# Kernel optimization log

Measured on AMD Instinct MI355X. Metric: run time of the kernel, lower is better.

Reference implementation:

```python
import jax, jax.numpy as jnp
import numpy as np

DIMS = [14400, 7200, 3600, 1800, 900, 450]  # in_dim then floor(dim/2) per layer
K = 25
BATCH = 256
NSTEPS = 10
OUT_DIM = 2


def setup_inputs() -> dict:
    key = jax.random.key(0)
    ks = jax.random.split(key, 13)
    inp = {"input": jax.random.normal(ks[0], (BATCH, NSTEPS, DIMS[0]), dtype=jnp.float32)}
    w_scale = (2.0 / K) ** 0.5  # matches normal_(0, (2/K)**0.5) init
    for i in range(5):
        d_prev, d = DIMS[i], DIMS[i + 1]
        inp[f"knn{i}"] = jax.random.randint(ks[1 + i], (d, K), 0, d_prev)
        inp[f"w{i}"] = w_scale * jax.random.normal(ks[6 + i], (d, K), dtype=jnp.float32)
        inp[f"b{i}"] = jnp.zeros((1, d), dtype=jnp.float32)
    inp["fc_w"] = jax.random.normal(ks[11], (OUT_DIM, DIMS[-1]), dtype=jnp.float32) * (1.0 / DIMS[-1] ** 0.5)
    inp["fc_b"] = jnp.zeros((OUT_DIM,), dtype=jnp.float32)
    return inp


def reference(input, knn0, knn1, knn2, knn3, knn4,
              w0, w1, w2, w3, w4, b0, b1, b2, b3, b4, fc_w, fc_b):
    # Faithful to the torch module: the synapses/membranes dicts are never
    # reassigned inside the step loop, so every snntorch Synaptic call sees
    # zero state: reset = Heaviside(0 - thr) = 0, syn = alpha*0 + I = I,
    # mem = beta*0 + syn = I.  The returned mem (x) is therefore exactly the
    # layer drive, there is no cross-step recurrence, and `angles` is
    # overwritten each step, so only the final timestep reaches the output.
    knns = (knn0, knn1, knn2, knn3, knn4)
    ws = (w0, w1, w2, w3, w4)
    bs = (b0, b1, b2, b3, b4)
    x = input[:, -1, :]  # [B, in_dim] -- last step (permute(1,0,2) then input[step])
    for knn, w, b in zip(knns, ws, bs):
        # gather KNN inputs [B, dim, K], weight locally, reduce over K, add bias
        x = jnp.einsum('bdk,dk->bd', x[:, knn], w) + b
    angles = x @ fc_w.T + fc_b  # fc_angle
    return angles  # (mem4_rec, spk4_rec are empty lists in the original)
```

## Files before the change

### kernel.cpp

```cpp
#include <hip/hip_runtime.h>

#define NSTEPS 10
#define D_IN   14400
#define KNN_K  25

#define L0D 7200
#define L1D 3600
#define L2D 1800
#define L3D 900
#define L4D 450
#define NROWS 13950

#define G0 113
#define G1 57
#define G2 29
#define G3 15
#define G4 8
#define SPG 832
#define O1 (G0*SPG)
#define O2 (O1 + G1*SPG)
#define O3 (O2 + G2*SPG)
#define O4 (O3 + G3*SPG)
#define OTOT (O4 + G4*SPG)

#define NPAIR 128
#define NPACK (NPAIR * (D_IN/4))

#define SPLIT0 3584

__device__ __forceinline__ unsigned bf16b(float x) {
    unsigned u = __float_as_uint(x);
    return (u + 0x7fffu + ((u >> 16) & 1u)) >> 16;
}

__device__ __forceinline__ void gpairB(unsigned u, const char* __restrict__ actb,
                                       float& s0, float& s1) {
    unsigned av = *(const unsigned*)(actb + (u & 0xffffu));
    float wf = __uint_as_float(u & 0xffff0000u);
    s0 = fmaf(__uint_as_float(av << 16),          wf, s0);
    s1 = fmaf(__uint_as_float(av & 0xffff0000u),  wf, s1);
}

__global__ void prep_kernel(const int* __restrict__ k0, const float* __restrict__ w0,
                            const int* __restrict__ k1, const float* __restrict__ w1,
                            const int* __restrict__ k2, const float* __restrict__ w2,
                            const int* __restrict__ k3, const float* __restrict__ w3,
                            const int* __restrict__ k4, const float* __restrict__ w4,
                            const float* __restrict__ input,
                            uint2* __restrict__ tile, uint4* __restrict__ xpk)
{
    const int s = blockIdx.x * 256 + threadIdx.x;
    if (s < NROWS) {
        const int* kp; const float* wp; int dl, obase;
        if      (s < L0D)             { kp = k0; wp = w0; dl = s;         obase = 0;  }
        else if (s < L0D+L1D)         { kp = k1; wp = w1; dl = s - L0D;   obase = O1; }
        else if (s < L0D+L1D+L2D)     { kp = k2; wp = w2; dl = s-L0D-L1D; obase = O2; }
        else if (s < L0D+L1D+L2D+L3D) { kp = k3; wp = w3; dl = s-L0D-L1D-L2D; obase = O3; }
        else                          { kp = k4; wp = w4; dl = s-L0D-L1D-L2D-L3D; obase = O4; }
        const int g = dl >> 6, l = dl & 63;

        int   idx[KNN_K]; float wv[KNN_K]; int bk[KNN_K];
#pragma unroll
        for (int k = 0; k < KNN_K; ++k) {
            idx[k] = kp[dl * KNN_K + k];
            wv[k]  = wp[dl * KNN_K + k];
            bk[k]  = idx[k] & 31;
        }
        const int lm = l - (l >= 50 ? 50 : (l >= 25 ? 25 : 0));
        unsigned* tw = (unsigned*)tile + 2u * (unsigned)(obase + g * SPG);
#pragma unroll
        for (int k = 0; k < KNN_K; ++k) {
            int rank = 0;
#pragma unroll
            for (int j = 0; j < KNN_K; ++j)
                rank += (bk[j] < bk[k]) || (bk[j] == bk[k] && j < k);
            int slot = rank + lm; if (slot >= KNN_K) slot -= KNN_K;
            unsigned u = (bf16b(wv[k]) << 16) | ((unsigned)idx[k] << 2);
            tw[((slot >> 1) * 64 + l) * 2 + (slot & 1)] = u;
        }
        tw[(12 * 64 + l) * 2 + 1] = 0;
        return;
    }
    const int t = s - NROWS;
    if (t < NPACK) {
        const int p = t / (D_IN / 4);
        const int c = t - p * (D_IN / 4);
        const float4 a = *(const float4*)(input + ((size_t)(2*p)   * NSTEPS + NSTEPS-1) * D_IN + 4*c);
        const float4 b = *(const float4*)(input + ((size_t)(2*p+1) * NSTEPS + NSTEPS-1) * D_IN + 4*c);
        uint4 wd;
        wd.x = bf16b(a.x) | (bf16b(b.x) << 16);
        wd.y = bf16b(a.y) | (bf16b(b.y) << 16);
        wd.z = bf16b(a.z) | (bf16b(b.z) << 16);
        wd.w = bf16b(a.w) | (bf16b(b.w) << 16);
        xpk[(size_t)p * (D_IN / 4) + c] = wd;
    }
}

__global__ __launch_bounds__(512, 2)
void lcn_l0(const uint4* __restrict__ xpk, const uint2* __restrict__ tile,
            const float* __restrict__ bias0, unsigned* __restrict__ y0)
{
    __shared__ unsigned act[D_IN];
    const int tid = threadIdx.x;
    const int p   = blockIdx.x & 127;
    const int h   = blockIdx.x >> 7;

    const uint4* src = xpk + (size_t)p * (D_IN / 4);
    for (int i = tid; i < D_IN / 4; i += 512)
        *(uint4*)(act + i * 4) = src[i];
    __syncthreads();
    const char* actb = (const char*)act;

    const int rbase = h ? SPLIT0 : 0;
    const int rend  = h ? L0D    : SPLIT0;
#pragma unroll
    for (int i = 0; i < 8; ++i) {
        int r = rbase + tid + i * 512;
        if (r < rend) {
            const uint2* tp = tile + (size_t)(r >> 6) * SPG + (r & 63);
            float a = bias0[r], b = a, c = 0.f, d = 0.f;
#pragma unroll
            for (int j = 0; j < 13; ++j) {
                uint2 u = tp[j * 64];
                gpairB(u.x, actb, a, b);
                gpairB(u.y, actb, c, d);
            }
            a += c; b += d;
            y0[(size_t)p * L0D + r] = bf16b(a) | (bf16b(b) << 16);
        }
    }
}

template<int DIM>
__device__ __forceinline__ void glayerT(const char* __restrict__ actb,
                                        unsigned* __restrict__ yout,
                                        const uint2* __restrict__ tb,
                                        const float* __restrict__ bias, int tid)
{
#pragma unroll
    for (int i = 0; i < (DIM + 1023) / 1024; ++i) {
        int r = tid + i * 1024;
        if (r < DIM) {
            const uint2* tp = tb + (size_t)(r >> 6) * SPG + (r & 63);
            float a = bias[r], b = a, c = 0.f, d = 0.f;
#pragma unroll
            for (int j = 0; j < 13; ++j) {
                uint2 u = tp[j * 64];
                gpairB(u.x, actb, a, b);
                gpairB(u.y, actb, c, d);
            }
            a += c; b += d;
            yout[r] = bf16b(a) | (bf16b(b) << 16);
        }
    }
}

__global__ __launch_bounds__(1024)
void lcn_tail(const unsigned* __restrict__ y0, const uint2* __restrict__ tile,
              const float* __restrict__ b1, const float* __restrict__ b2,
              const float* __restrict__ b3, const float* __restrict__ b4,
              const float* __restrict__ fc_w, const float* __restrict__ fc_b,
              float* __restrict__ out)
{
    __shared__ unsigned sm[L0D + L1D];
    const int tid = threadIdx.x;
    const int p   = blockIdx.x;

    const uint4* src = (const uint4*)(y0 + (size_t)p * L0D);
    for (int i = tid; i < L0D / 4; i += 1024)
        *(uint4*)(sm + 4 * i) = src[i];
    __syncthreads();

    glayerT<L1D>((const char*)sm,         sm + L0D,        tile + O1, b1, tid);
    __syncthreads();
    glayerT<L2D>((const char*)(sm + L0D), sm,              tile + O2, b2, tid);
    __syncthreads();
    glayerT<L3D>((const char*)sm,         sm + L2D,        tile + O3, b3, tid);
    __syncthreads();
    glayerT<L4D>((const char*)(sm + L2D), sm + L2D + L3D,  tile + O4, b4, tid);
    __syncthreads();

    const unsigned* C = sm + L2D + L3D;
    if (tid < 256) {
        const int wv = tid >> 6, lane = tid & 63;
        const int o = wv >> 1, j = wv & 1;
        float s = 0.f;
#pragma unroll
        for (int it = 0; it < 8; ++it) {
            int r = lane + it * 64;
            if (r < L4D) {
                unsigned av = C[r];
                unsigned hbits = j ? (av & 0xffff0000u) : (av << 16);
                s += __uint_as_float(hbits) * fc_w[o * L4D + r];
            }
        }
#pragma unroll
        for (int off = 32; off > 0; off >>= 1) s += __shfl_xor(s, off);
        if (lane == 0) out[(2 * p + j) * 2 + o] = s + fc_b[o];
    }
}

extern "C" void kernel_launch(void* const* d_in, const int* in_sizes, int n_in,
                              void* d_out, int out_size, void* d_ws, size_t ws_size,
                              hipStream_t stream) {
    const float* input = (const float*)d_in[0];
    const int*   knn[5];
    const float* w[5];
    const float* bias[5];
    for (int i = 0; i < 5; ++i) {
        knn[i]  = (const int*)  d_in[1 + 3 * i];
        w[i]    = (const float*)d_in[2 + 3 * i];
        bias[i] = (const float*)d_in[3 + 3 * i];
    }
    const float* fc_w = (const float*)d_in[16];
    const float* fc_b = (const float*)d_in[17];
    float* out = (float*)d_out;

    char* base = (char*)d_ws;
    uint2*    tile = (uint2*)base;
    uint4*    xpk  = (uint4*)(base + (size_t)OTOT * 8);
    unsigned* y0   = (unsigned*)((char*)xpk + (size_t)NPAIR * D_IN * 4);

    const int nprep = NROWS + NPACK;
    prep_kernel<<<(nprep + 255) / 256, 256, 0, stream>>>(
        knn[0], w[0], knn[1], w[1], knn[2], w[2], knn[3], w[3], knn[4], w[4],
        input, tile, xpk);

    lcn_l0<<<256, 512, 0, stream>>>(xpk, tile, bias[0], y0);

    lcn_tail<<<NPAIR, 1024, 0, stream>>>(y0, tile, bias[1], bias[2], bias[3], bias[4],
                                         fc_w, fc_b, out);
}
```

Before: 40.77 us.

## Split layer 1 into its own 256-block kernel and switch packing to fp16

Layer 1 moves out of the single 128-block tail kernel into its own kernel that runs 256 half-blocks, like layer 0. The tail kernel also runs 256 blocks, each redundantly computing layers 2-4 for a sample pair but keeping only one half for the FC output. The aim is to use more of the GPU's compute units during the tail layers. Activations and weights are now packed as fp16 instead of bf16, which changes the conversion cost and precision. In exchange there is an extra kernel launch and a round trip of y1 through global memory.

```diff
diff --git a/kernel.cpp b/kernel.cpp
--- a/kernel.cpp
+++ b/kernel.cpp
@@ -1,4 +1,5 @@
 #include <hip/hip_runtime.h>
+#include <hip/hip_fp16.h>
 
 #define NSTEPS 10
 #define D_IN   14400
@@ -27,18 +28,18 @@
 #define NPACK (NPAIR * (D_IN/4))
 
 #define SPLIT0 3584
-
-__device__ __forceinline__ unsigned bf16b(float x) {
-    unsigned u = __float_as_uint(x);
-    return (u + 0x7fffu + ((u >> 16) & 1u)) >> 16;
-}
-
-__device__ __forceinline__ void gpairB(unsigned u, const char* __restrict__ actb,
-                                       float& s0, float& s1) {
-    unsigned av = *(const unsigned*)(actb + (u & 0xffffu));
-    float wf = __uint_as_float(u & 0xffff0000u);
-    s0 = fmaf(__uint_as_float(av << 16),          wf, s0);
-    s1 = fmaf(__uint_as_float(av & 0xffff0000u),  wf, s1);
+#define SPLIT1 1792
+
+__device__ __forceinline__ unsigned f16b(float x) {
+    return (unsigned)__half_as_ushort(__float2half_rn(x));
+}
+
+__device__ __forceinline__ void gh2(unsigned u, const char* __restrict__ actb,
+                                    float& s0, float& s1) {
+    const __half2 av = *(const __half2*)(actb + (u & 0xffffu));
+    const __half  wh = __ushort_as_half((unsigned short)(u >> 16));
+    s0 = fmaf(__half2float(__low2half(av)),  __half2float(wh), s0);
+    s1 = fmaf(__half2float(__high2half(av)), __half2float(wh), s1);
 }
 
 __global__ void prep_kernel(const int* __restrict__ k0, const float* __restrict__ w0,
@@ -52,14 +53,14 @@
     const int s = blockIdx.x * 256 + threadIdx.x;
     if (s < NROWS) {
         const int* kp; const float* wp; int dl, obase;
-        if      (s < L0D)             { kp = k0; wp = w0; dl = s;         obase = 0;  }
-        else if (s < L0D+L1D)         { kp = k1; wp = w1; dl = s - L0D;   obase = O1; }
-        else if (s < L0D+L1D+L2D)     { kp = k2; wp = w2; dl = s-L0D-L1D; obase = O2; }
+        if      (s < L0D)             { kp = k0; wp = w0; dl = s;             obase = 0;  }
+        else if (s < L0D+L1D)         { kp = k1; wp = w1; dl = s - L0D;       obase = O1; }
+        else if (s < L0D+L1D+L2D)     { kp = k2; wp = w2; dl = s-L0D-L1D;     obase = O2; }
         else if (s < L0D+L1D+L2D+L3D) { kp = k3; wp = w3; dl = s-L0D-L1D-L2D; obase = O3; }
         else                          { kp = k4; wp = w4; dl = s-L0D-L1D-L2D-L3D; obase = O4; }
         const int g = dl >> 6, l = dl & 63;
 
-        int   idx[KNN_K]; float wv[KNN_K]; int bk[KNN_K];
+        int idx[KNN_K]; float wv[KNN_K]; int bk[KNN_K];
 #pragma unroll
         for (int k = 0; k < KNN_K; ++k) {
             idx[k] = kp[dl * KNN_K + k];
@@ -75,7 +76,7 @@
             for (int j = 0; j < KNN_K; ++j)
                 rank += (bk[j] < bk[k]) || (bk[j] == bk[k] && j < k);
             int slot = rank + lm; if (slot >= KNN_K) slot -= KNN_K;
-            unsigned u = (bf16b(wv[k]) << 16) | ((unsigned)idx[k] << 2);
+            unsigned u = (f16b(wv[k]) << 16) | ((unsigned)idx[k] << 2);
             tw[((slot >> 1) * 64 + l) * 2 + (slot & 1)] = u;
         }
         tw[(12 * 64 + l) * 2 + 1] = 0;
@@ -88,17 +89,42 @@
         const float4 a = *(const float4*)(input + ((size_t)(2*p)   * NSTEPS + NSTEPS-1) * D_IN + 4*c);
         const float4 b = *(const float4*)(input + ((size_t)(2*p+1) * NSTEPS + NSTEPS-1) * D_IN + 4*c);
         uint4 wd;
-        wd.x = bf16b(a.x) | (bf16b(b.x) << 16);
-        wd.y = bf16b(a.y) | (bf16b(b.y) << 16);
-        wd.z = bf16b(a.z) | (bf16b(b.z) << 16);
-        wd.w = bf16b(a.w) | (bf16b(b.w) << 16);
+        wd.x = f16b(a.x) | (f16b(b.x) << 16);
+        wd.y = f16b(a.y) | (f16b(b.y) << 16);
+        wd.z = f16b(a.z) | (f16b(b.z) << 16);
+        wd.w = f16b(a.w) | (f16b(b.w) << 16);
         xpk[(size_t)p * (D_IN / 4) + c] = wd;
+    }
+}
+
+template<int MAXI, int BLK>
+__device__ __forceinline__ void glayerG(const char* __restrict__ actb,
+                                        unsigned* __restrict__ yout,
+                                        const uint2* __restrict__ tb,
+                                        const float* __restrict__ bias,
+                                        int lo, int hi, int tid)
+{
+#pragma unroll
+    for (int i = 0; i < MAXI; ++i) {
+        int r = lo + tid + i * BLK;
+        if (r < hi) {
+            const uint2* tp = tb + (size_t)(r >> 6) * SPG + (r & 63);
+            float a0 = bias[r], a1 = a0, c0 = 0.f, c1 = 0.f;
+#pragma unroll
+            for (int j = 0; j < 13; ++j) {
+                uint2 u = tp[j * 64];
+                gh2(u.x, actb, a0, a1);
+                gh2(u.y, actb, c0, c1);
+            }
+            a0 += c0; a1 += c1;
+            yout[r] = f16b(a0) | (f16b(a1) << 16);
+        }
     }
 }
 
 __global__ __launch_bounds__(512, 2)
 void lcn_l0(const uint4* __restrict__ xpk, const uint2* __restrict__ tile,
-            const float* __restrict__ bias0, unsigned* __restrict__ y0)
+            const float* __restrict__ b0, unsigned* __restrict__ y0)
 {
     __shared__ unsigned act[D_IN];
     const int tid = threadIdx.x;
@@ -107,96 +133,78 @@
 
     const uint4* src = xpk + (size_t)p * (D_IN / 4);
     for (int i = tid; i < D_IN / 4; i += 512)
-        *(uint4*)(act + i * 4) = src[i];
-    __syncthreads();
-    const char* actb = (const char*)act;
-
-    const int rbase = h ? SPLIT0 : 0;
-    const int rend  = h ? L0D    : SPLIT0;
-#pragma unroll
-    for (int i = 0; i < 8; ++i) {
-        int r = rbase + tid + i * 512;
-        if (r < rend) {
-            const uint2* tp = tile + (size_t)(r >> 6) * SPG + (r & 63);
-            float a = bias0[r], b = a, c = 0.f, d = 0.f;
-#pragma unroll
-            for (int j = 0; j < 13; ++j) {
-                uint2 u = tp[j * 64];
-                gpairB(u.x, actb, a, b);
-                gpairB(u.y, actb, c, d);
-            }
-            a += c; b += d;
-            y0[(size_t)p * L0D + r] = bf16b(a) | (bf16b(b) << 16);
-        }
-    }
-}
-
-template<int DIM>
-__device__ __forceinline__ void glayerT(const char* __restrict__ actb,
-                                        unsigned* __restrict__ yout,
-                                        const uint2* __restrict__ tb,
-                                        const float* __restrict__ bias, int tid)
-{
-#pragma unroll
-    for (int i = 0; i < (DIM + 1023) / 1024; ++i) {
-        int r = tid + i * 1024;
-        if (r < DIM) {
-            const uint2* tp = tb + (size_t)(r >> 6) * SPG + (r & 63);
-            float a = bias[r], b = a, c = 0.f, d = 0.f;
-#pragma unroll
-            for (int j = 0; j < 13; ++j) {
-                uint2 u = tp[j * 64];
-                gpairB(u.x, actb, a, b);
-                gpairB(u.y, actb, c, d);
-            }
-            a += c; b += d;
-            yout[r] = bf16b(a) | (bf16b(b) << 16);
-        }
-    }
+        *(uint4*)(act + 4 * i) = src[i];
+    __syncthreads();
+
+    glayerG<8, 512>((const char*)act, y0 + (size_t)p * L0D, tile, b0,
+                    h ? SPLIT0 : 0, h ? L0D : SPLIT0, tid);
+}
+
+__global__ __launch_bounds__(512, 2)
+void lcn_l1(const unsigned* __restrict__ y0, const uint2* __restrict__ tile,
+            const float* __restrict__ b1, unsigned* __restrict__ y1)
+{
+    __shared__ unsigned act[L0D];
+    const int tid = threadIdx.x;
+    const int p   = blockIdx.x & 127;
+    const int h   = blockIdx.x >> 7;
+
+    const uint4* src = (const uint4*)(y0 + (size_t)p * L0D);
+    for (int i = tid; i < L0D / 4; i += 512)
+        *(uint4*)(act + 4 * i) = src[i];
+    __syncthreads();
+
+    glayerG<4, 512>((const char*)act, y1 + (size_t)p * L1D, tile + O1, b1,
+                    h ? SPLIT1 : 0, h ? L1D : SPLIT1, tid);
 }
 
 __global__ __launch_bounds__(1024)
-void lcn_tail(const unsigned* __restrict__ y0, const uint2* __restrict__ tile,
-              const float* __restrict__ b1, const float* __restrict__ b2,
-              const float* __restrict__ b3, const float* __restrict__ b4,
+void lcn_tail(const unsigned* __restrict__ y1, const uint2* __restrict__ tile,
+              const float* __restrict__ b2, const float* __restrict__ b3,
+              const float* __restrict__ b4,
               const float* __restrict__ fc_w, const float* __restrict__ fc_b,
               float* __restrict__ out)
 {
-    __shared__ unsigned sm[L0D + L1D];
+    __shared__ unsigned sm[L1D + L2D + L3D];
+    __shared__ float y4[L4D];
     const int tid = threadIdx.x;
-    const int p   = blockIdx.x;
-
-    const uint4* src = (const uint4*)(y0 + (size_t)p * L0D);
-    for (int i = tid; i < L0D / 4; i += 1024)
-        *(uint4*)(sm + 4 * i) = src[i];
-    __syncthreads();
-
-    glayerT<L1D>((const char*)sm,         sm + L0D,        tile + O1, b1, tid);
-    __syncthreads();
-    glayerT<L2D>((const char*)(sm + L0D), sm,              tile + O2, b2, tid);
-    __syncthreads();
-    glayerT<L3D>((const char*)sm,         sm + L2D,        tile + O3, b3, tid);
-    __syncthreads();
-    glayerT<L4D>((const char*)(sm + L2D), sm + L2D + L3D,  tile + O4, b4, tid);
-    __syncthreads();
-
-    const unsigned* C = sm + L2D + L3D;
-    if (tid < 256) {
-        const int wv = tid >> 6, lane = tid & 63;
-        const int o = wv >> 1, j = wv & 1;
+    const int p   = blockIdx.x & 127;
+    const int h   = blockIdx.x >> 7;
+
+    const uint4* src = (const uint4*)(y1 + (size_t)p * L1D);
+    if (tid < L1D / 4) *(uint4*)(sm + 4 * tid) = src[tid];
+    __syncthreads();
+
+    glayerG<2, 1024>((const char*)sm, sm + L1D, tile + O2, b2, 0, L2D, tid);
+    __syncthreads();
+    glayerG<1, 1024>((const char*)(sm + L1D), sm + L1D + L2D, tile + O3, b3, 0, L3D, tid);
+    __syncthreads();
+    if (tid < L4D) {
+        const uint2* tp = tile + O4 + (size_t)(tid >> 6) * SPG + (tid & 63);
+        const char* actb = (const char*)(sm + L1D + L2D);
+        float a0 = b4[tid], a1 = a0, c0 = 0.f, c1 = 0.f;
+#pragma unroll
+        for (int j = 0; j < 13; ++j) {
+            uint2 u = tp[j * 64];
+            gh2(u.x, actb, a0, a1);
+            gh2(u.y, actb, c0, c1);
+        }
+        a0 += c0; a1 += c1;
+        y4[tid] = h ? a1 : a0;
+    }
+    __syncthreads();
+
+    if (tid < 128) {
+        const int o = tid >> 6, lane = tid & 63;
         float s = 0.f;
 #pragma unroll
         for (int it = 0; it < 8; ++it) {
             int r = lane + it * 64;
-            if (r < L4D) {
-                unsigned av = C[r];
-                unsigned hbits = j ? (av & 0xffff0000u) : (av << 16);
-                s += __uint_as_float(hbits) * fc_w[o * L4D + r];
-            }
+            if (r < L4D) s += y4[r] * fc_w[o * L4D + r];
         }
 #pragma unroll
         for (int off = 32; off > 0; off >>= 1) s += __shfl_xor(s, off);
-        if (lane == 0) out[(2 * p + j) * 2 + o] = s + fc_b[o];
+        if (lane == 0) out[(2 * p + h) * 2 + o] = s + fc_b[o];
     }
 }
 
@@ -220,6 +228,7 @@
     uint2*    tile = (uint2*)base;
     uint4*    xpk  = (uint4*)(base + (size_t)OTOT * 8);
     unsigned* y0   = (unsigned*)((char*)xpk + (size_t)NPAIR * D_IN * 4);
+    unsigned* y1   = y0 + (size_t)NPAIR * L0D;
 
     const int nprep = NROWS + NPACK;
     prep_kernel<<<(nprep + 255) / 256, 256, 0, stream>>>(
@@ -227,7 +236,7 @@
         input, tile, xpk);
 
     lcn_l0<<<256, 512, 0, stream>>>(xpk, tile, bias[0], y0);
-
-    lcn_tail<<<NPAIR, 1024, 0, stream>>>(y0, tile, bias[1], bias[2], bias[3], bias[4],
-                                         fc_w, fc_b, out);
-}
+    lcn_l1<<<256, 512, 0, stream>>>(y0, tile, bias[1], y1);
+    lcn_tail<<<256, 1024, 0, stream>>>(y1, tile, bias[2], bias[3], bias[4],
+                                       fc_w, fc_b, out);
+}
```

Result: slower. 42.00 us (+3.0%).
